# Performance work log

Hardware: AMD Instinct MI355X
Metric: run time of the kernel (lower is better)

The kernel has to match this reference:

```python
import jax, jax.numpy as jnp
import numpy as np

WS = 7
HEADS = 8
DIM = 256
IN_DIM = 128
HID = 1024
EPS = 1e-5


def _rel_index(ws):
    coords = np.stack(np.meshgrid(np.arange(ws), np.arange(ws), indexing='ij'))  # (2,ws,ws)
    cf = coords.reshape(2, -1)                      # (2,N)
    rel = (cf[:, :, None] - cf[:, None, :]).transpose(1, 2, 0).copy()  # (N,N,2)
    rel[..., 0] += ws - 1
    rel[..., 1] += ws - 1
    rel[..., 0] *= 2 * ws - 1
    return rel.sum(-1)  # (N,N) int

REL_IDX = jnp.asarray(_rel_index(WS).reshape(-1))


def layernorm(x, g, b):
    mu = jnp.mean(x, axis=-1, keepdims=True)
    var = jnp.mean(jnp.square(x - mu), axis=-1, keepdims=True)
    return (x - mu) * jax.lax.rsqrt(var + EPS) * g + b


def setup_inputs() -> dict:
    key = jax.random.key(0)
    ks = jax.random.split(key, 16)
    s = 0.02
    return {
        'x': jax.random.normal(ks[0], (16, IN_DIM, 56, 56), jnp.float32),
        'conv_w': jax.random.normal(ks[1], (DIM, IN_DIM, 3, 3), jnp.float32) * s,
        'conv_b': jnp.zeros((DIM,), jnp.float32),
        'g1': jnp.ones((DIM,), jnp.float32), 'b1': jnp.zeros((DIM,), jnp.float32),
        'g2': jnp.ones((DIM,), jnp.float32), 'b2': jnp.zeros((DIM,), jnp.float32),
        'g3': jnp.ones((DIM,), jnp.float32), 'b3': jnp.zeros((DIM,), jnp.float32),
        'qkv_w': jax.random.normal(ks[2], (3 * DIM, DIM), jnp.float32) * s,
        'rel_bias_table': jax.random.normal(ks[3], ((2 * WS - 1) ** 2, HEADS), jnp.float32) * s,
        'proj_w': jax.random.normal(ks[4], (DIM, DIM), jnp.float32) * s,
        'proj_b': jnp.zeros((DIM,), jnp.float32),
        'fc1_w': jax.random.normal(ks[5], (HID, DIM), jnp.float32) * s,
        'fc1_b': jnp.zeros((HID,), jnp.float32),
        'fc2_w': jax.random.normal(ks[6], (DIM, HID), jnp.float32) * s,
        'fc2_b': jnp.zeros((DIM,), jnp.float32),
    }


def reference(x, conv_w, conv_b, g1, b1, g2, b2, g3, b3, qkv_w, rel_bias_table,
              proj_w, proj_b, fc1_w, fc1_b, fc2_w, fc2_b):
    # proj_q: 3x3 conv, stride 1, pad 1 (input_dim != embed_dim)
    x = jax.lax.conv_general_dilated(
        x, conv_w, window_strides=(1, 1), padding=((1, 1), (1, 1)),
        dimension_numbers=('NCHW', 'OIHW', 'NCHW')) + conv_b[None, :, None, None]
    b, c, h, w = x.shape
    x = x.reshape(b, c, h * w).transpose(0, 2, 1)  # (b, n, c)
    x = layernorm(x, g1, b1)
    x = x.reshape(b, h, w, c)
    pb = (WS - h % WS) % WS
    pr = (WS - w % WS) % WS
    x = jnp.pad(x, ((0, 0), (0, pb), (0, pr), (0, 0)))
    hp, wp = h + pb, w + pr
    # window partition -> (nW, N, c)
    xw = x.reshape(b, hp // WS, WS, wp // WS, WS, c)
    xw = xw.transpose(0, 1, 3, 2, 4, 5).reshape(-1, WS * WS, c)
    nW, N, _ = xw.shape
    d = c // HEADS
    qkv = (xw @ qkv_w.T).reshape(nW, N, 3, HEADS, d).transpose(2, 0, 3, 1, 4)  # (3,nW,h,N,d)
    q, k, v = qkv[0] * (d ** -0.5), qkv[1], qkv[2]
    attn = jnp.einsum('whnd,whmd->whnm', q, k)
    bias = rel_bias_table[REL_IDX].reshape(N, N, HEADS).transpose(2, 0, 1)  # (h,N,N)
    attn = jax.nn.softmax(attn + bias[None], axis=-1)
    out = jnp.einsum('whnm,whmd->whnd', attn, v).transpose(0, 2, 1, 3).reshape(nW, N, c)
    out = out @ proj_w.T + proj_b
    # window reverse
    x = out.reshape(b, hp // WS, wp // WS, WS, WS, c)
    x = x.transpose(0, 1, 3, 2, 4, 5).reshape(b, hp, wp, c)
    x = x[:, :h, :w, :].reshape(b, h * w, c)
    # NOTE: faithful to source — NO residual from pre-attention stream
    x = layernorm(x, g2, b2)
    x = jax.nn.gelu(x @ fc1_w.T + fc1_b, approximate=False) @ fc2_w.T + fc2_b
    x = x + x  # source: x = x + drop_path(x) with identity drop_path
    x = layernorm(x, g3, b3)
    return x.reshape(b, h, w, c).transpose(0, 3, 1, 2)
```

## Files before the change

kernel.cpp:

```cpp
#include <hip/hip_runtime.h>
#include <hip/hip_bf16.h>

typedef unsigned short u16;
typedef unsigned int   u32;

#define TTOK  50176
#define CDIM  256

using short8 = __attribute__((ext_vector_type(8))) short;
using f32x4  = __attribute__((ext_vector_type(4))) float;

__device__ __forceinline__ float b2f(u16 u) { return __uint_as_float(((u32)u) << 16); }
__device__ __forceinline__ u16 f2b(float f) {
    u32 x = __float_as_uint(f);
    return (u16)((x + 0x7fffu + ((x >> 16) & 1u)) >> 16);
}

#define GLD16(src, dst) __builtin_amdgcn_global_load_lds( \
    (const __attribute__((address_space(1))) void*)(src),  \
    (__attribute__((address_space(3))) void*)(dst), 16, 0, 0)

__global__ __launch_bounds__(256) void cvt4_k(const float* __restrict__ a, const float* __restrict__ b,
                                              const float* __restrict__ c, const float* __restrict__ d,
                                              u16* __restrict__ dst) {
    int i = blockIdx.x * 256 + threadIdx.x;
    const float* src; int off;
    if (i < 49152)       { src = a; off = i; }
    else if (i < 65536)  { src = b; off = i - 49152; }
    else if (i < 131072) { src = c; off = i - 65536; }
    else                 { src = d; off = i - 131072; }
    float4 v = *(const float4*)&src[off * 4];
    ushort4 o;
    o.x = f2b(v.x); o.y = f2b(v.y); o.z = f2b(v.z); o.w = f2b(v.w);
    *(ushort4*)&dst[i * 4] = o;
}

__global__ __launch_bounds__(256) void pad_k(const float* __restrict__ x, u16* __restrict__ xp) {
    __shared__ float tile[128][58];
    int bid = blockIdx.x;
    int b = bid / 58, hp = bid - b * 58;
    int tid = threadIdx.x;
    bool zrow = (hp == 0 || hp == 57);
    if (!zrow) {
        int h = hp - 1;
        for (int e = tid; e < 128 * 14; e += 256) {
            int ic = e / 14, j = e - ic * 14;
            float4 v = *(const float4*)&x[(((size_t)b * 128 + ic) * 56 + h) * 56 + j * 4];
            tile[ic][j * 4 + 0] = v.x; tile[ic][j * 4 + 1] = v.y;
            tile[ic][j * 4 + 2] = v.z; tile[ic][j * 4 + 3] = v.w;
        }
        __syncthreads();
    }
    size_t rb = ((size_t)b * 58 + hp) * 58 * 128;
    for (int u = tid; u < 58 * 16; u += 256) {
        int wp = u / 16, icg = u - wp * 16;
        uint4 o = make_uint4(0u, 0u, 0u, 0u);
        if (!zrow && wp != 0 && wp != 57) {
            int w = wp - 1, ic0 = icg * 8;
            u16 v0 = f2b(tile[ic0 + 0][w]), v1 = f2b(tile[ic0 + 1][w]);
            u16 v2 = f2b(tile[ic0 + 2][w]), v3 = f2b(tile[ic0 + 3][w]);
            u16 v4 = f2b(tile[ic0 + 4][w]), v5 = f2b(tile[ic0 + 5][w]);
            u16 v6 = f2b(tile[ic0 + 6][w]), v7 = f2b(tile[ic0 + 7][w]);
            o.x = (u32)v0 | ((u32)v1 << 16);
            o.y = (u32)v2 | ((u32)v3 << 16);
            o.z = (u32)v4 | ((u32)v5 << 16);
            o.w = (u32)v6 | ((u32)v7 << 16);
        }
        *(uint4*)&xp[rb + (size_t)wp * 128 + icg * 8] = o;
    }
}

__global__ __launch_bounds__(256) void w2_k(const float* __restrict__ w, u16* __restrict__ o2) {
    int e = blockIdx.x * 256 + threadIdx.x;
    int o = e / 1152, rem = e - o * 1152;
    int tap = rem >> 7, ic = rem & 127;
    o2[e] = f2b(w[(o * 128 + ic) * 9 + tap]);
}

__device__ __forceinline__ void xcd_remap(int& bx, int& by) {
    int nx = gridDim.x, ny = gridDim.y;
    if ((ny & 7) == 0) {
        int linear = blockIdx.y * nx + blockIdx.x;
        int xcd = linear & 7, within = linear >> 3;
        bx = within % nx;
        by = xcd * (ny >> 3) + within / nx;
    } else { bx = blockIdx.x; by = blockIdx.y; }
}

__device__ __forceinline__ int xcd_remap1d() {
    int nb = gridDim.x, lin = blockIdx.x;
    int q = nb >> 3, r = nb & 7;
    int xcd = lin & 7, idx = lin >> 3;
    return (xcd < r ? xcd * (q + 1) : r * (q + 1) + (xcd - r) * q) + idx;
}

__global__ __launch_bounds__(256) void gemm_conv_ln_k(const u16* __restrict__ xp, const u16* __restrict__ W2,
                                                      const float* __restrict__ bias,
                                                      const float* __restrict__ gam, const float* __restrict__ bet,
                                                      u16* __restrict__ C) {
    __shared__ __align__(16) u16 lsA[2][64 * 32];
    __shared__ __align__(16) u16 lsB[2][256 * 32];
    int tid = threadIdx.x;
    int wave = tid >> 6, lane = tid & 63;
    int by = xcd_remap1d();
    int mBase = by * 64;
    int wm = wave >> 1, wn = wave & 1;
    int lr = lane & 15, lq = lane >> 4;
    int rr4 = lane >> 2, kc = lane & 3;
    int kcs = (kc ^ ((rr4 >> 1) & 3)) * 8;

    size_t tbA;
    {
        int t = mBase + wave * 16 + rr4;
        int win = t / 49, n = t - win * 49;
        int b = win >> 6, wh = (win >> 3) & 7, ww = win & 7;
        int r = n / 7, s = n - r * 7;
        tbA = ((size_t)(b * 58 + wh * 7 + r) * 58 + ww * 7 + s) * 128 + kcs;
    }
    const u16* gB[4];
#pragma unroll
    for (int j = 0; j < 4; ++j)
        gB[j] = W2 + (size_t)(j * 64 + wave * 16 + rr4) * 1152 + kcs;

    f32x4 acc[2][8];
#pragma unroll
    for (int m = 0; m < 2; ++m)
#pragma unroll
        for (int n = 0; n < 8; ++n) acc[m][n] = (f32x4){0.f, 0.f, 0.f, 0.f};

#define CONV_STAGE(ks, buf) do { \
        int tap_ = (ks) >> 2, qz_ = (ks) & 3; \
        int kh_ = tap_ / 3, kw_ = tap_ - kh_ * 3; \
        GLD16(xp + tbA + (kh_ * 58 + kw_) * 128 + qz_ * 32, &lsA[buf][(wave * 16 + rr4) * 32]); \
        _Pragma("unroll") \
        for (int j_ = 0; j_ < 4; ++j_) \
            GLD16(gB[j_] + (ks) * 32, &lsB[buf][(j_ * 64 + wave * 16 + rr4) * 32]); \
    } while (0)

    CONV_STAGE(0, 0);
    __syncthreads();
    int slq = (lq ^ ((lr >> 1) & 3)) * 8;
    for (int ks = 0; ks < 36; ++ks) {
        int cur = ks & 1;
        if (ks + 1 < 36) CONV_STAGE(ks + 1, cur ^ 1);
        short8 af[2], bf[8];
#pragma unroll
        for (int m = 0; m < 2; ++m)
            af[m] = *(const short8*)&lsA[cur][(wm * 32 + m * 16 + lr) * 32 + slq];
#pragma unroll
        for (int n = 0; n < 8; ++n)
            bf[n] = *(const short8*)&lsB[cur][(wn * 128 + n * 16 + lr) * 32 + slq];
#pragma unroll
        for (int m = 0; m < 2; ++m)
#pragma unroll
            for (int n = 0; n < 8; ++n)
                acc[m][n] = __builtin_amdgcn_mfma_f32_16x16x32_bf16(af[m], bf[n], acc[m][n], 0, 0, 0);
        __syncthreads();
    }
#undef CONV_STAGE

    float bv[8], gv[8], btv[8];
#pragma unroll
    for (int n = 0; n < 8; ++n) {
        int col = wn * 128 + n * 16 + lr;
        bv[n] = bias[col]; gv[n] = gam[col]; btv[n] = bet[col];
    }
#pragma unroll
    for (int m = 0; m < 2; ++m)
#pragma unroll
        for (int n = 0; n < 8; ++n)
#pragma unroll
            for (int r = 0; r < 4; ++r) acc[m][n][r] += bv[n];

    float* red = (float*)lsA;
#pragma unroll
    for (int m = 0; m < 2; ++m)
#pragma unroll
        for (int r = 0; r < 4; ++r) {
            float s = 0.f, qq = 0.f;
#pragma unroll
            for (int n = 0; n < 8; ++n) { float v = acc[m][n][r]; s += v; qq += v * v; }
            s += __shfl_xor(s, 1); s += __shfl_xor(s, 2); s += __shfl_xor(s, 4); s += __shfl_xor(s, 8);
            qq += __shfl_xor(qq, 1); qq += __shfl_xor(qq, 2); qq += __shfl_xor(qq, 4); qq += __shfl_xor(qq, 8);
            if (lr == 0) {
                int row = wm * 32 + m * 16 + lq * 4 + r;
                red[row * 4 + wn * 2] = s; red[row * 4 + wn * 2 + 1] = qq;
            }
        }
    __syncthreads();

#pragma unroll
    for (int m = 0; m < 2; ++m)
#pragma unroll
        for (int r = 0; r < 4; ++r) {
            int row = wm * 32 + m * 16 + lq * 4 + r;
            float S = red[row * 4] + red[row * 4 + 2];
            float Q = red[row * 4 + 1] + red[row * 4 + 3];
            float mean = S * (1.f / 256.f);
            float var = Q * (1.f / 256.f) - mean * mean;
            float inv = rsqrtf(var + 1e-5f);
            size_t grow = (size_t)(mBase + row) * 256;
#pragma unroll
            for (int n = 0; n < 8; ++n) {
                int col = wn * 128 + n * 16 + lr;
                C[grow + col] = f2b((acc[m][n][r] - mean) * inv * gv[n] + btv[n]);
            }
        }
}

__global__ __launch_bounds__(256) void gemm_ln_k(const u16* __restrict__ A, const u16* __restrict__ Bw,
                                                 const float* __restrict__ bias,
                                                 const float* __restrict__ gam, const float* __restrict__ bet,
                                                 u16* __restrict__ C, int K) {
    __shared__ __align__(16) u16 lsA[2][64 * 32];
    __shared__ __align__(16) u16 lsB[2][256 * 32];
    int tid = threadIdx.x;
    int wave = tid >> 6, lane = tid & 63;
    int by = xcd_remap1d();
    int mBase = by * 64;
    int wm = wave >> 1, wn = wave & 1;
    int lr = lane & 15, lq = lane >> 4;
    int rr4 = lane >> 2, kc = lane & 3;
    int kcs = (kc ^ ((rr4 >> 1) & 3)) * 8;

    const u16* gA = A + (size_t)(mBase + wave * 16 + rr4) * K + kcs;
    const u16* gB[4];
#pragma unroll
    for (int j = 0; j < 4; ++j)
        gB[j] = Bw + (size_t)(j * 64 + wave * 16 + rr4) * K + kcs;

    f32x4 acc[2][8];
#pragma unroll
    for (int m = 0; m < 2; ++m)
#pragma unroll
        for (int n = 0; n < 8; ++n) acc[m][n] = (f32x4){0.f, 0.f, 0.f, 0.f};

#define LN_STAGE(ks, buf) do { \
        GLD16(gA + (ks) * 32, &lsA[buf][(wave * 16 + rr4) * 32]); \
        _Pragma("unroll") \
        for (int j_ = 0; j_ < 4; ++j_) \
            GLD16(gB[j_] + (ks) * 32, &lsB[buf][(j_ * 64 + wave * 16 + rr4) * 32]); \
    } while (0)

    int nk = K >> 5;
    LN_STAGE(0, 0);
    __syncthreads();
    int slq = (lq ^ ((lr >> 1) & 3)) * 8;
    for (int ks = 0; ks < nk; ++ks) {
        int cur = ks & 1;
        if (ks + 1 < nk) LN_STAGE(ks + 1, cur ^ 1);
        short8 af[2], bf[8];
#pragma unroll
        for (int m = 0; m < 2; ++m)
            af[m] = *(const short8*)&lsA[cur][(wm * 32 + m * 16 + lr) * 32 + slq];
#pragma unroll
        for (int n = 0; n < 8; ++n)
            bf[n] = *(const short8*)&lsB[cur][(wn * 128 + n * 16 + lr) * 32 + slq];
#pragma unroll
        for (int m = 0; m < 2; ++m)
#pragma unroll
            for (int n = 0; n < 8; ++n)
                acc[m][n] = __builtin_amdgcn_mfma_f32_16x16x32_bf16(af[m], bf[n], acc[m][n], 0, 0, 0);
        __syncthreads();
    }
#undef LN_STAGE

    float bv[8], gv[8], btv[8];
#pragma unroll
    for (int n = 0; n < 8; ++n) {
        int col = wn * 128 + n * 16 + lr;
        bv[n] = bias[col]; gv[n] = gam[col]; btv[n] = bet[col];
    }
#pragma unroll
    for (int m = 0; m < 2; ++m)
#pragma unroll
        for (int n = 0; n < 8; ++n)
#pragma unroll
            for (int r = 0; r < 4; ++r) acc[m][n][r] += bv[n];

    float* red = (float*)lsA;
#pragma unroll
    for (int m = 0; m < 2; ++m)
#pragma unroll
        for (int r = 0; r < 4; ++r) {
            float s = 0.f, qq = 0.f;
#pragma unroll
            for (int n = 0; n < 8; ++n) { float v = acc[m][n][r]; s += v; qq += v * v; }
            s += __shfl_xor(s, 1); s += __shfl_xor(s, 2); s += __shfl_xor(s, 4); s += __shfl_xor(s, 8);
            qq += __shfl_xor(qq, 1); qq += __shfl_xor(qq, 2); qq += __shfl_xor(qq, 4); qq += __shfl_xor(qq, 8);
            if (lr == 0) {
                int row = wm * 32 + m * 16 + lq * 4 + r;
                red[row * 4 + wn * 2] = s; red[row * 4 + wn * 2 + 1] = qq;
            }
        }
    __syncthreads();

#pragma unroll
    for (int m = 0; m < 2; ++m)
#pragma unroll
        for (int r = 0; r < 4; ++r) {
            int row = wm * 32 + m * 16 + lq * 4 + r;
            float S = red[row * 4] + red[row * 4 + 2];
            float Q = red[row * 4 + 1] + red[row * 4 + 3];
            float mean = S * (1.f / 256.f);
            float var = Q * (1.f / 256.f) - mean * mean;
            float inv = rsqrtf(var + 1e-5f);
            size_t grow = (size_t)(mBase + row) * 256;
#pragma unroll
            for (int n = 0; n < 8; ++n) {
                int col = wn * 128 + n * 16 + lr;
                C[grow + col] = f2b((acc[m][n][r] - mean) * inv * gv[n] + btv[n]);
            }
        }
}

template <int EPI>
__global__ __launch_bounds__(256) void gemm_k(const u16* __restrict__ A, const u16* __restrict__ Bw,
                                              const float* __restrict__ bias, u16* __restrict__ C,
                                              int M, int N, int K) {
    __shared__ __align__(16) u16 lsA[2][128 * 32];
    __shared__ __align__(16) u16 lsB[2][128 * 32];
    int tid = threadIdx.x;
    int wave = tid >> 6, lane = tid & 63;
    int bx, by; xcd_remap(bx, by);
    int mBase = by * 128, nBase = bx * 128;
    int wm = wave >> 1, wn = wave & 1;
    int lr = lane & 15, lq = lane >> 4;
    int rr = lane >> 2, kc = lane & 3;
    int kcs = (kc ^ ((rr >> 1) & 3)) * 8;

    const u16* gA[2]; const u16* gB[2];
#pragma unroll
    for (int j = 0; j < 2; ++j) {
        int row = wave * 32 + j * 16 + rr;
        gA[j] = A  + (size_t)(mBase + row) * K + kcs;
        gB[j] = Bw + (size_t)(nBase + row) * K + kcs;
    }

    f32x4 acc[4][4];
#pragma unroll
    for (int m = 0; m < 4; ++m)
#pragma unroll
        for (int n = 0; n < 4; ++n) acc[m][n] = (f32x4){0.f, 0.f, 0.f, 0.f};

    int nk = K >> 5;
#pragma unroll
    for (int j = 0; j < 2; ++j) {
        GLD16(gA[j], &lsA[0][(wave * 32 + j * 16) * 32]);
        GLD16(gB[j], &lsB[0][(wave * 32 + j * 16) * 32]);
    }
    __syncthreads();

    int slq = (lq ^ ((lr >> 1) & 3)) * 8;
    for (int ks = 0; ks < nk; ++ks) {
        int cur = ks & 1;
        if (ks + 1 < nk) {
            int nxt = cur ^ 1;
            int ko = (ks + 1) << 5;
#pragma unroll
            for (int j = 0; j < 2; ++j) {
                GLD16(gA[j] + ko, &lsA[nxt][(wave * 32 + j * 16) * 32]);
                GLD16(gB[j] + ko, &lsB[nxt][(wave * 32 + j * 16) * 32]);
            }
        }
        short8 af[4], bf[4];
#pragma unroll
        for (int m = 0; m < 4; ++m)
            af[m] = *(const short8*)&lsA[cur][(wm * 64 + m * 16 + lr) * 32 + slq];
#pragma unroll
        for (int n = 0; n < 4; ++n)
            bf[n] = *(const short8*)&lsB[cur][(wn * 64 + n * 16 + lr) * 32 + slq];
#pragma unroll
        for (int m = 0; m < 4; ++m)
#pragma unroll
            for (int n = 0; n < 4; ++n)
                acc[m][n] = __builtin_amdgcn_mfma_f32_16x16x32_bf16(bf[n], af[m], acc[m][n], 0, 0, 0);
        __syncthreads();
    }

#pragma unroll
    for (int m = 0; m < 4; ++m) {
        int row = mBase + wm * 64 + m * 16 + lr;
        u16* crow = C + (size_t)row * N;
#pragma unroll
        for (int n = 0; n < 4; ++n) {
            int col0 = nBase + wn * 64 + n * 16 + lq * 4;
            float b0 = 0.f, b1 = 0.f, b2 = 0.f, b3 = 0.f;
            if (EPI >= 1) {
                float4 bv4 = *(const float4*)&bias[col0];
                b0 = bv4.x; b1 = bv4.y; b2 = bv4.z; b3 = bv4.w;
            }
            float v0 = acc[m][n][0] + b0, v1 = acc[m][n][1] + b1;
            float v2 = acc[m][n][2] + b2, v3 = acc[m][n][3] + b3;
            if (EPI == 2) {
                float u0 = 0.79788456f * (v0 + 0.044715f * v0 * v0 * v0);
                float u1 = 0.79788456f * (v1 + 0.044715f * v1 * v1 * v1);
                float u2 = 0.79788456f * (v2 + 0.044715f * v2 * v2 * v2);
                float u3 = 0.79788456f * (v3 + 0.044715f * v3 * v3 * v3);
                v0 = v0 * __frcp_rn(1.f + __expf(-2.f * u0));
                v1 = v1 * __frcp_rn(1.f + __expf(-2.f * u1));
                v2 = v2 * __frcp_rn(1.f + __expf(-2.f * u2));
                v3 = v3 * __frcp_rn(1.f + __expf(-2.f * u3));
            }
            ushort4 o;
            o.x = f2b(v0); o.y = f2b(v1); o.z = f2b(v2); o.w = f2b(v3);
            *(ushort4*)&crow[col0] = o;
        }
    }
}

__global__ __launch_bounds__(256) void attn_mfma_k(const u16* __restrict__ qkv,
                                                   const float* __restrict__ tab,
                                                   u16* __restrict__ out) {
    __shared__ __align__(16) u16 sh[28488];
    int tid = threadIdx.x;
    int wave = tid >> 6, lane = tid & 63;
    int wh = blockIdx.x * 4 + wave;
    int win = wh >> 3, head = wh & 7;
    int g = lane >> 4, cc = lane & 15;

    u16* Pl = sh + wave * 4608;
    u16* Vl = sh + 18432 + wave * 2176;
    float* bs = (float*)(sh + 27136) + wave * 169;

    const size_t wbase = (size_t)win * 49 * 768;
    for (int e = lane; e < 169; e += 64) bs[e] = tab[e * 8 + head];
    for (int e = lane; e < 49 * 16; e += 64) {
        int k = e >> 4, d0 = (e & 15) * 2;
        *(u32*)&Vl[k * 34 + d0] = *(const u32*)&qkv[wbase + (size_t)k * 768 + 512 + head * 32 + d0];
    }
    for (int e = lane; e < 15 * 16; e += 64) {
        int k = 49 + (e >> 4), d0 = (e & 15) * 2;
        *(u32*)&Vl[k * 34 + d0] = 0u;
    }
    __syncthreads();

    short8 aQ[4], bK[4];
#pragma unroll
    for (int t = 0; t < 4; ++t) {
        int qr = t * 16 + cc; if (qr > 48) qr = 48;
        aQ[t] = *(const short8*)&qkv[wbase + (size_t)qr * 768 + head * 32 + g * 8];
        int kr = t * 16 + cc; if (kr > 48) kr = 48;
        bK[t] = *(const short8*)&qkv[wbase + (size_t)kr * 768 + 256 + head * 32 + g * 8];
    }
    f32x4 S[4][4];
#pragma unroll
    for (int a = 0; a < 4; ++a)
#pragma unroll
        for (int b = 0; b < 4; ++b)
            S[a][b] = __builtin_amdgcn_mfma_f32_16x16x32_bf16(aQ[a], bK[b], (f32x4){0.f,0.f,0.f,0.f}, 0, 0, 0);

    int AqA[4][4];
#pragma unroll
    for (int tr = 0; tr < 4; ++tr)
#pragma unroll
        for (int r = 0; r < 4; ++r) {
            int q = tr * 16 + g * 4 + r; if (q > 48) q = 48;
            int dq = (q * 37) >> 8;
            AqA[tr][r] = 6 * dq + q + 84;
        }
    int AcA[4];
    bool colBad[4];
#pragma unroll
    for (int tc = 0; tc < 4; ++tc) {
        int c = tc * 16 + cc;
        colBad[tc] = (c > 48);
        if (c > 48) c = 48;
        int dc = (c * 37) >> 8;
        AcA[tc] = 6 * dc + c;
    }
    const float scale = 0.17677669529663687f;
    float inv[4][4];
#pragma unroll
    for (int tr = 0; tr < 4; ++tr) {
#pragma unroll
        for (int r = 0; r < 4; ++r) {
            float z0 = colBad[0] ? -1e30f : S[tr][0][r] * scale + bs[AqA[tr][r] - AcA[0]];
            float z1 = colBad[1] ? -1e30f : S[tr][1][r] * scale + bs[AqA[tr][r] - AcA[1]];
            float z2 = colBad[2] ? -1e30f : S[tr][2][r] * scale + bs[AqA[tr][r] - AcA[2]];
            float z3 = colBad[3] ? -1e30f : S[tr][3][r] * scale + bs[AqA[tr][r] - AcA[3]];
            float mx = fmaxf(fmaxf(z0, z1), fmaxf(z2, z3));
            mx = fmaxf(mx, __shfl_xor(mx, 1));
            mx = fmaxf(mx, __shfl_xor(mx, 2));
            mx = fmaxf(mx, __shfl_xor(mx, 4));
            mx = fmaxf(mx, __shfl_xor(mx, 8));
            float p0 = __expf(z0 - mx), p1 = __expf(z1 - mx);
            float p2 = __expf(z2 - mx), p3 = __expf(z3 - mx);
            S[tr][0][r] = p0; S[tr][1][r] = p1; S[tr][2][r] = p2; S[tr][3][r] = p3;
            float sm = p0 + p1 + p2 + p3;
            sm += __shfl_xor(sm, 1); sm += __shfl_xor(sm, 2);
            sm += __shfl_xor(sm, 4); sm += __shfl_xor(sm, 8);
            inv[tr][r] = 1.0f / sm;
        }
    }

#pragma unroll
    for (int tr = 0; tr < 4; ++tr)
#pragma unroll
        for (int tc = 0; tc < 4; ++tc) {
            int k = tc * 16 + cc;
            u16* pb = &Pl[tr * 1152 + k * 18 + g * 4];
            u32 w0 = (u32)f2b(S[tr][tc][0]) | ((u32)f2b(S[tr][tc][1]) << 16);
            u32 w1 = (u32)f2b(S[tr][tc][2]) | ((u32)f2b(S[tr][tc][3]) << 16);
            *(u32*)pb = w0;
            *(u32*)(pb + 2) = w1;
        }
    __syncthreads();

    f32x4 O[4][2];
#pragma unroll
    for (int a = 0; a < 4; ++a) { O[a][0] = (f32x4){0.f,0.f,0.f,0.f}; O[a][1] = (f32x4){0.f,0.f,0.f,0.f}; }
#pragma unroll
    for (int s = 0; s < 2; ++s) {
        short8 pa[4], vb[2];
#pragma unroll
        for (int tr = 0; tr < 4; ++tr)
#pragma unroll
            for (int j = 0; j < 8; ++j)
                pa[tr][j] = (short)Pl[tr * 1152 + (s * 32 + g * 8 + j) * 18 + cc];
#pragma unroll
        for (int td = 0; td < 2; ++td)
#pragma unroll
            for (int j = 0; j < 8; ++j)
                vb[td][j] = (short)Vl[(s * 32 + g * 8 + j) * 34 + td * 16 + cc];
#pragma unroll
        for (int tr = 0; tr < 4; ++tr)
#pragma unroll
            for (int td = 0; td < 2; ++td)
                O[tr][td] = __builtin_amdgcn_mfma_f32_16x16x32_bf16(pa[tr], vb[td], O[tr][td], 0, 0, 0);
    }

#pragma unroll
    for (int tr = 0; tr < 4; ++tr)
#pragma unroll
        for (int r = 0; r < 4; ++r) {
            int q = tr * 16 + g * 4 + r;
            if (q < 49) {
                float iv = inv[tr][r];
                u16* op = out + (size_t)(win * 49 + q) * 256 + head * 32;
                op[cc]      = f2b(O[tr][0][r] * iv);
                op[16 + cc] = f2b(O[tr][1][r] * iv);
            }
        }
}

__global__ __launch_bounds__(256) void ln3_out_k(const u16* __restrict__ f, const float* __restrict__ g3,
                                                 const float* __restrict__ b3, float* __restrict__ out) {
    __shared__ float tile[256][57];
    int bh = blockIdx.x;
    int b = bh / 56, h = bh - b * 56;
    int wv = threadIdx.x >> 6, lane = threadIdx.x & 63;
    int wh = h / 7, r = h - wh * 7;
    float4 gg = *(const float4*)&g3[lane * 4];
    float4 bb = *(const float4*)&b3[lane * 4];
    for (int i = 0; i < 14; ++i) {
        int w = wv + i * 4;
        int wwn = w / 7, s2 = w - wwn * 7;
        int t = (b * 64 + wh * 8 + wwn) * 49 + r * 7 + s2;
        ushort4 u = *(const ushort4*)&f[(size_t)t * 256 + lane * 4];
        float v0 = 2.f * b2f(u.x), v1 = 2.f * b2f(u.y), v2 = 2.f * b2f(u.z), v3 = 2.f * b2f(u.w);
        float s = v0 + v1 + v2 + v3;
        float q = v0 * v0 + v1 * v1 + v2 * v2 + v3 * v3;
#pragma unroll
        for (int o = 32; o; o >>= 1) { s += __shfl_xor(s, o); q += __shfl_xor(q, o); }
        float mean = s * (1.f / 256.f);
        float var = q * (1.f / 256.f) - mean * mean;
        float inv = rsqrtf(var + 1e-5f);
        int c = lane * 4;
        tile[c + 0][w] = (v0 - mean) * inv * gg.x + bb.x;
        tile[c + 1][w] = (v1 - mean) * inv * gg.y + bb.y;
        tile[c + 2][w] = (v2 - mean) * inv * gg.z + bb.z;
        tile[c + 3][w] = (v3 - mean) * inv * gg.w + bb.w;
    }
    __syncthreads();
    size_t obase = (size_t)b * 256 * 3136 + (size_t)h * 56;
#pragma unroll
    for (int it = 0; it < 28; ++it) {
        int e = it * 256 + threadIdx.x;
        int c = e / 28, wu = e - c * 28;
        float2 pack = make_float2(tile[c][wu * 2], tile[c][wu * 2 + 1]);
        *(float2*)&out[obase + (size_t)c * 3136 + wu * 2] = pack;
    }
}

extern "C" void kernel_launch(void* const* d_in, const int* in_sizes, int n_in,
                              void* d_out, int out_size, void* d_ws, size_t ws_size,
                              hipStream_t stream) {
    (void)in_sizes; (void)n_in; (void)out_size;
    const float* x      = (const float*)d_in[0];
    const float* conv_w = (const float*)d_in[1];
    const float* conv_b = (const float*)d_in[2];
    const float* g1     = (const float*)d_in[3];
    const float* b1     = (const float*)d_in[4];
    const float* g2     = (const float*)d_in[5];
    const float* b2     = (const float*)d_in[6];
    const float* g3     = (const float*)d_in[7];
    const float* b3     = (const float*)d_in[8];
    const float* qkv_w  = (const float*)d_in[9];
    const float* tab    = (const float*)d_in[10];
    const float* proj_w = (const float*)d_in[11];
    const float* proj_b = (const float*)d_in[12];
    const float* fc1_w  = (const float*)d_in[13];
    const float* fc1_b  = (const float*)d_in[14];
    const float* fc2_w  = (const float*)d_in[15];
    const float* fc2_b  = (const float*)d_in[16];
    float* outp = (float*)d_out;

    const size_t OFF_Y  = (size_t)TTOK * 1152 * 2;
    const size_t OFF_AT = OFF_Y + (size_t)TTOK * 512;
    const size_t NEED   = OFF_AT + (size_t)TTOK * 512;
    if (ws_size < NEED) return;

    char* ws = (char*)d_ws;
    u16* xpad    = (u16*)ws;
    u16* ybuf    = (u16*)(ws + OFF_Y);
    u16* atout   = (u16*)(ws + OFF_AT);
    u16* qkvbuf  = (u16*)ws;
    u16* hidden  = (u16*)ws;
    u16* W2      = atout;
    u16* wbase   = (u16*)(ws + (size_t)TTOK * 1024 * 2);
    u16* qkvw_b  = wbase;
    u16* projw_b = wbase + 196608;
    u16* fc1w_b  = projw_b + 65536;
    u16* fc2w_b  = fc1w_b + 262144;

    pad_k<<<928, 256, 0, stream>>>(x, xpad);
    w2_k<<<1152, 256, 0, stream>>>(conv_w, W2);
    cvt4_k<<<768, 256, 0, stream>>>(qkv_w, proj_w, fc1_w, fc2_w, qkvw_b);
    gemm_conv_ln_k<<<784, 256, 0, stream>>>(xpad, W2, conv_b, g1, b1, ybuf);
    gemm_k<0><<<dim3(6, 392), 256, 0, stream>>>(ybuf, qkvw_b, nullptr, qkvbuf, TTOK, 768, 256);
    attn_mfma_k<<<2048, 256, 0, stream>>>(qkvbuf, tab, atout);
    gemm_ln_k<<<784, 256, 0, stream>>>(atout, projw_b, proj_b, g2, b2, ybuf, 256);
    gemm_k<2><<<dim3(8, 392), 256, 0, stream>>>(ybuf, fc1w_b, fc1_b, hidden, TTOK, 1024, 256);
    gemm_k<1><<<dim3(2, 392), 256, 0, stream>>>(hidden, fc2w_b, fc2_b, atout, TTOK, 256, 1024);
    ln3_out_k<<<896, 256, 0, stream>>>(atout, g3, b3, outp);
}
```

Measured before the change: 373.0 us.

## Merge prep kernels, swap MFMA operand order, use scalar epilogue stores

The three preprocessing kernels (input pad/cast, conv weight reorder, linear weight cast) are merged into one launch that dispatches on block index, removing two kernel launches. The bf16 rounding helper now uses the HIP intrinsic. The global_load_lds LDS destinations drop the per-lane row offset so each wave passes a uniform base. In the generic GEMM the MFMA operands are swapped, so each lane holds four rows of one column, and the epilogue now writes scalar bf16 values with a scalar bias load. The scalar stores are narrower and less coalesced than the previous 8-byte vector stores, which could raise write cost on the large fc1 hidden output.

New measurement: 333.2 us. 10.7% less time.

```diff
diff --git a/kernel.cpp b/kernel.cpp
--- a/kernel.cpp
+++ b/kernel.cpp
@@ -12,69 +12,70 @@
 
 __device__ __forceinline__ float b2f(u16 u) { return __uint_as_float(((u32)u) << 16); }
 __device__ __forceinline__ u16 f2b(float f) {
-    u32 x = __float_as_uint(f);
-    return (u16)((x + 0x7fffu + ((x >> 16) & 1u)) >> 16);
+    union { __hip_bfloat16 h; u16 u; } cv;
+    cv.h = __float2bfloat16(f);
+    return cv.u;
 }
 
 #define GLD16(src, dst) __builtin_amdgcn_global_load_lds( \
     (const __attribute__((address_space(1))) void*)(src),  \
     (__attribute__((address_space(3))) void*)(dst), 16, 0, 0)
 
-__global__ __launch_bounds__(256) void cvt4_k(const float* __restrict__ a, const float* __restrict__ b,
-                                              const float* __restrict__ c, const float* __restrict__ d,
-                                              u16* __restrict__ dst) {
-    int i = blockIdx.x * 256 + threadIdx.x;
-    const float* src; int off;
-    if (i < 49152)       { src = a; off = i; }
-    else if (i < 65536)  { src = b; off = i - 49152; }
-    else if (i < 131072) { src = c; off = i - 65536; }
-    else                 { src = d; off = i - 131072; }
-    float4 v = *(const float4*)&src[off * 4];
-    ushort4 o;
-    o.x = f2b(v.x); o.y = f2b(v.y); o.z = f2b(v.z); o.w = f2b(v.w);
-    *(ushort4*)&dst[i * 4] = o;
-}
-
-__global__ __launch_bounds__(256) void pad_k(const float* __restrict__ x, u16* __restrict__ xp) {
+__global__ __launch_bounds__(256) void prep_k(const float* __restrict__ x, u16* __restrict__ xp,
+                                              const float* __restrict__ cw, u16* __restrict__ W2,
+                                              const float* __restrict__ qw, const float* __restrict__ pw,
+                                              const float* __restrict__ f1w, const float* __restrict__ f2w,
+                                              u16* __restrict__ wdst) {
     __shared__ float tile[128][58];
     int bid = blockIdx.x;
-    int b = bid / 58, hp = bid - b * 58;
     int tid = threadIdx.x;
-    bool zrow = (hp == 0 || hp == 57);
-    if (!zrow) {
-        int h = hp - 1;
-        for (int e = tid; e < 128 * 14; e += 256) {
-            int ic = e / 14, j = e - ic * 14;
-            float4 v = *(const float4*)&x[(((size_t)b * 128 + ic) * 56 + h) * 56 + j * 4];
-            tile[ic][j * 4 + 0] = v.x; tile[ic][j * 4 + 1] = v.y;
-            tile[ic][j * 4 + 2] = v.z; tile[ic][j * 4 + 3] = v.w;
-        }
-        __syncthreads();
-    }
-    size_t rb = ((size_t)b * 58 + hp) * 58 * 128;
-    for (int u = tid; u < 58 * 16; u += 256) {
-        int wp = u / 16, icg = u - wp * 16;
-        uint4 o = make_uint4(0u, 0u, 0u, 0u);
-        if (!zrow && wp != 0 && wp != 57) {
-            int w = wp - 1, ic0 = icg * 8;
-            u16 v0 = f2b(tile[ic0 + 0][w]), v1 = f2b(tile[ic0 + 1][w]);
-            u16 v2 = f2b(tile[ic0 + 2][w]), v3 = f2b(tile[ic0 + 3][w]);
-            u16 v4 = f2b(tile[ic0 + 4][w]), v5 = f2b(tile[ic0 + 5][w]);
-            u16 v6 = f2b(tile[ic0 + 6][w]), v7 = f2b(tile[ic0 + 7][w]);
-            o.x = (u32)v0 | ((u32)v1 << 16);
-            o.y = (u32)v2 | ((u32)v3 << 16);
-            o.z = (u32)v4 | ((u32)v5 << 16);
-            o.w = (u32)v6 | ((u32)v7 << 16);
-        }
-        *(uint4*)&xp[rb + (size_t)wp * 128 + icg * 8] = o;
-    }
-}
-
-__global__ __launch_bounds__(256) void w2_k(const float* __restrict__ w, u16* __restrict__ o2) {
-    int e = blockIdx.x * 256 + threadIdx.x;
-    int o = e / 1152, rem = e - o * 1152;
-    int tap = rem >> 7, ic = rem & 127;
-    o2[e] = f2b(w[(o * 128 + ic) * 9 + tap]);
+    if (bid < 928) {
+        int b = bid / 58, hp = bid - b * 58;
+        bool zrow = (hp == 0 || hp == 57);
+        if (!zrow) {
+            int h = hp - 1;
+            for (int e = tid; e < 128 * 14; e += 256) {
+                int ic = e / 14, j = e - ic * 14;
+                float4 v = *(const float4*)&x[(((size_t)b * 128 + ic) * 56 + h) * 56 + j * 4];
+                tile[ic][j * 4 + 0] = v.x; tile[ic][j * 4 + 1] = v.y;
+                tile[ic][j * 4 + 2] = v.z; tile[ic][j * 4 + 3] = v.w;
+            }
+            __syncthreads();
+        }
+        size_t rb = ((size_t)b * 58 + hp) * 58 * 128;
+        for (int u = tid; u < 58 * 16; u += 256) {
+            int wp = u / 16, icg = u - wp * 16;
+            uint4 o = make_uint4(0u, 0u, 0u, 0u);
+            if (!zrow && wp != 0 && wp != 57) {
+                int w = wp - 1, ic0 = icg * 8;
+                u16 v0 = f2b(tile[ic0 + 0][w]), v1 = f2b(tile[ic0 + 1][w]);
+                u16 v2 = f2b(tile[ic0 + 2][w]), v3 = f2b(tile[ic0 + 3][w]);
+                u16 v4 = f2b(tile[ic0 + 4][w]), v5 = f2b(tile[ic0 + 5][w]);
+                u16 v6 = f2b(tile[ic0 + 6][w]), v7 = f2b(tile[ic0 + 7][w]);
+                o.x = (u32)v0 | ((u32)v1 << 16);
+                o.y = (u32)v2 | ((u32)v3 << 16);
+                o.z = (u32)v4 | ((u32)v5 << 16);
+                o.w = (u32)v6 | ((u32)v7 << 16);
+            }
+            *(uint4*)&xp[rb + (size_t)wp * 128 + icg * 8] = o;
+        }
+    } else if (bid < 2080) {
+        int e = (bid - 928) * 256 + tid;
+        int o = e / 1152, rem = e - o * 1152;
+        int tap = rem >> 7, ic = rem & 127;
+        W2[e] = f2b(cw[(o * 128 + ic) * 9 + tap]);
+    } else {
+        int i = (bid - 2080) * 256 + tid;
+        const float* src; int off;
+        if (i < 49152)       { src = qw;  off = i; }
+        else if (i < 65536)  { src = pw;  off = i - 49152; }
+        else if (i < 131072) { src = f1w; off = i - 65536; }
+        else                 { src = f2w; off = i - 131072; }
+        float4 v = *(const float4*)&src[off * 4];
+        ushort4 o;
+        o.x = f2b(v.x); o.y = f2b(v.y); o.z = f2b(v.z); o.w = f2b(v.w);
+        *(ushort4*)&wdst[i * 4] = o;
+    }
 }
 
 __device__ __forceinline__ void xcd_remap(int& bx, int& by) {
@@ -131,10 +132,10 @@
 #define CONV_STAGE(ks, buf) do { \
         int tap_ = (ks) >> 2, qz_ = (ks) & 3; \
         int kh_ = tap_ / 3, kw_ = tap_ - kh_ * 3; \
-        GLD16(xp + tbA + (kh_ * 58 + kw_) * 128 + qz_ * 32, &lsA[buf][(wave * 16 + rr4) * 32]); \
+        GLD16(xp + tbA + (kh_ * 58 + kw_) * 128 + qz_ * 32, &lsA[buf][(wave * 16) * 32]); \
         _Pragma("unroll") \
         for (int j_ = 0; j_ < 4; ++j_) \
-            GLD16(gB[j_] + (ks) * 32, &lsB[buf][(j_ * 64 + wave * 16 + rr4) * 32]); \
+            GLD16(gB[j_] + (ks) * 32, &lsB[buf][(j_ * 64 + wave * 16) * 32]); \
     } while (0)
 
     CONV_STAGE(0, 0);
@@ -236,10 +237,10 @@
         for (int n = 0; n < 8; ++n) acc[m][n] = (f32x4){0.f, 0.f, 0.f, 0.f};
 
 #define LN_STAGE(ks, buf) do { \
-        GLD16(gA + (ks) * 32, &lsA[buf][(wave * 16 + rr4) * 32]); \
+        GLD16(gA + (ks) * 32, &lsA[buf][(wave * 16) * 32]); \
         _Pragma("unroll") \
         for (int j_ = 0; j_ < 4; ++j_) \
-            GLD16(gB[j_] + (ks) * 32, &lsB[buf][(j_ * 64 + wave * 16 + rr4) * 32]); \
+            GLD16(gB[j_] + (ks) * 32, &lsB[buf][(j_ * 64 + wave * 16) * 32]); \
     } while (0)
 
     int nk = K >> 5;
@@ -374,37 +375,27 @@
         for (int m = 0; m < 4; ++m)
 #pragma unroll
             for (int n = 0; n < 4; ++n)
-                acc[m][n] = __builtin_amdgcn_mfma_f32_16x16x32_bf16(bf[n], af[m], acc[m][n], 0, 0, 0);
+                acc[m][n] = __builtin_amdgcn_mfma_f32_16x16x32_bf16(af[m], bf[n], acc[m][n], 0, 0, 0);
         __syncthreads();
     }
 
 #pragma unroll
     for (int m = 0; m < 4; ++m) {
-        int row = mBase + wm * 64 + m * 16 + lr;
-        u16* crow = C + (size_t)row * N;
+        int row0 = mBase + wm * 64 + m * 16 + lq * 4;
 #pragma unroll
         for (int n = 0; n < 4; ++n) {
-            int col0 = nBase + wn * 64 + n * 16 + lq * 4;
-            float b0 = 0.f, b1 = 0.f, b2 = 0.f, b3 = 0.f;
-            if (EPI >= 1) {
-                float4 bv4 = *(const float4*)&bias[col0];
-                b0 = bv4.x; b1 = bv4.y; b2 = bv4.z; b3 = bv4.w;
-            }
-            float v0 = acc[m][n][0] + b0, v1 = acc[m][n][1] + b1;
-            float v2 = acc[m][n][2] + b2, v3 = acc[m][n][3] + b3;
-            if (EPI == 2) {
-                float u0 = 0.79788456f * (v0 + 0.044715f * v0 * v0 * v0);
-                float u1 = 0.79788456f * (v1 + 0.044715f * v1 * v1 * v1);
-                float u2 = 0.79788456f * (v2 + 0.044715f * v2 * v2 * v2);
-                float u3 = 0.79788456f * (v3 + 0.044715f * v3 * v3 * v3);
-                v0 = v0 * __frcp_rn(1.f + __expf(-2.f * u0));
-                v1 = v1 * __frcp_rn(1.f + __expf(-2.f * u1));
-                v2 = v2 * __frcp_rn(1.f + __expf(-2.f * u2));
-                v3 = v3 * __frcp_rn(1.f + __expf(-2.f * u3));
-            }
-            ushort4 o;
-            o.x = f2b(v0); o.y = f2b(v1); o.z = f2b(v2); o.w = f2b(v3);
-            *(ushort4*)&crow[col0] = o;
+            int col = nBase + wn * 64 + n * 16 + lr;
+            float bv = (EPI >= 1) ? bias[col] : 0.f;
+#pragma unroll
+            for (int r = 0; r < 4; ++r) {
+                float v = acc[m][n][r] + bv;
+                if (EPI == 2) {
+                    float u = 0.79788456f * (v + 0.044715f * v * v * v);
+                    float e = __expf(-2.f * u);
+                    v = v * __frcp_rn(1.f + e);
+                }
+                C[(size_t)(row0 + r) * N + col] = f2b(v);
+            }
         }
     }
 }
@@ -624,9 +615,7 @@
     u16* fc1w_b  = projw_b + 65536;
     u16* fc2w_b  = fc1w_b + 262144;
 
-    pad_k<<<928, 256, 0, stream>>>(x, xpad);
-    w2_k<<<1152, 256, 0, stream>>>(conv_w, W2);
-    cvt4_k<<<768, 256, 0, stream>>>(qkv_w, proj_w, fc1_w, fc2_w, qkvw_b);
+    prep_k<<<2848, 256, 0, stream>>>(x, xpad, conv_w, W2, qkv_w, proj_w, fc1_w, fc2_w, qkvw_b);
     gemm_conv_ln_k<<<784, 256, 0, stream>>>(xpad, W2, conv_b, g1, b1, ybuf);
     gemm_k<0><<<dim3(6, 392), 256, 0, stream>>>(ybuf, qkvw_b, nullptr, qkvbuf, TTOK, 768, 256);
     attn_mfma_k<<<2048, 256, 0, stream>>>(qkvbuf, tab, atout);
```
